# Optimization experiments

Hardware: AMD Instinct MI355X
Metric: run time of the kernel (lower is better)

## Reference

```python
import jax, jax.numpy as jnp
import numpy as np
import math

B, S, D = 2, 2048, 1024
H, DK, DV = 16, 64, 64  # head_count, query_size, value_size; H*DV == D
NEG_INF = -jnp.inf


def setup_inputs() -> dict:
    key = jax.random.key(0)
    ks = jax.random.split(key, 10)
    sc = 0.02
    return {
        "input": jax.random.normal(ks[0], (B, S, D), dtype=jnp.float32),
        "padding_mask": jnp.zeros((B, S), dtype=jnp.float32),  # 0 = valid, 1 = padded
        "wq_w": jax.random.normal(ks[1], (H * DK, D), dtype=jnp.float32) * sc,
        "wq_b": jnp.zeros((H * DK,), dtype=jnp.float32),
        "wk_w": jax.random.normal(ks[2], (H * DK, D), dtype=jnp.float32) * sc,
        "wk_b": jnp.zeros((H * DK,), dtype=jnp.float32),
        "wv_w": jax.random.normal(ks[3], (H * DV, D), dtype=jnp.float32) * sc,
        "wv_b": jnp.zeros((H * DV,), dtype=jnp.float32),
        "fin_w": jax.random.normal(ks[4], (D, H * DV), dtype=jnp.float32) * sc,
        "fin_b": jnp.zeros((D,), dtype=jnp.float32),
    }


def reference(input, padding_mask, wq_w, wq_b, wk_w, wk_b, wv_w, wv_b, fin_w, fin_b):
    b, s, _ = input.shape
    # projections -> [b, h, s, d]
    Q = (input @ wq_w.T + wq_b).reshape(b, s, H, DK).transpose(0, 2, 1, 3)
    K = (input @ wk_w.T + wk_b).reshape(b, s, H, DK).transpose(0, 2, 1, 3)
    V = (input @ wv_w.T + wv_b).reshape(b, s, H, DV).transpose(0, 2, 1, 3)

    # padding mask: pad*(-inf), nan_to_num(0*inf -> 0); broadcast over query dim
    pad = jnp.where(padding_mask > 0, NEG_INF, 0.0)[:, None, None, :]  # [b,1,1,s]
    i = jnp.arange(s)
    causal = jnp.where(i[None, :] < i[:, None] + 1, 0.0, NEG_INF)  # [s,s]
    mask = pad + causal[None, None, :, :]

    # (QK^T + mask) / sqrt(dk), softmax over keys
    logits = (jnp.einsum("bhqd,bhkd->bhqk", Q, K) + mask) / math.sqrt(DK)
    attn = jax.nn.softmax(logits, axis=-1)
    out = jnp.einsum("bhqk,bhkd->bqhd", attn, V).reshape(b, s, H * DV)
    return out @ fin_w.T + fin_b
```

## Files before the change

kernel.cpp:

```cpp
#include <hip/hip_runtime.h>


typedef __bf16 bf16;
typedef __bf16 bf16x4 __attribute__((ext_vector_type(4)));
typedef __bf16 bf16x8 __attribute__((ext_vector_type(8)));
typedef float  f32x4  __attribute__((ext_vector_type(4)));

#define B_  2
#define S_  2048
#define D_  1024
#define H_  16
#define HD  64
#define NEG_BIG (-3.0e38f)
#define SCALE_LOG2E 0.1803368801111204f

#define NSPLIT_QT 14
#define SLOTS_PER_BH (2 * NSPLIT_QT)

__device__ __forceinline__ void lds16(const void* g, void* l) {
    __builtin_amdgcn_global_load_lds((const __attribute__((address_space(1))) void*)g,
                                     (__attribute__((address_space(3))) void*)l, 16, 0, 0);
}

__device__ __forceinline__ f32x4 mfma16(bf16x8 a, bf16x8 b, f32x4 c) {
    return __builtin_amdgcn_mfma_f32_16x16x32_bf16(a, b, c, 0, 0, 0);
}

#define IT(qt, k0, ke) ((uint32_t)(qt) | ((uint32_t)(k0) << 8) | ((uint32_t)(ke) << 16))
__device__ __constant__ uint32_t g_items[46] = {
    IT(16,0,9),  IT(17,0,9),
    IT(30,0,8),  IT(30,8,16), IT(31,0,8),  IT(31,8,16),
    IT(28,0,8),  IT(29,0,8),  IT(14,0,8),  IT(15,0,8),
    IT(28,8,15), IT(29,8,15), IT(26,0,7),  IT(26,7,14),
    IT(27,0,7),  IT(27,7,14), IT(24,0,7),  IT(25,0,7),
    IT(12,0,7),  IT(13,0,7),
    IT(24,7,13), IT(25,7,13), IT(22,0,6),  IT(22,6,12),
    IT(23,0,6),  IT(23,6,12), IT(20,0,6),  IT(21,0,6),
    IT(10,0,6),  IT(11,0,6),
    IT(20,6,11), IT(21,6,11), IT(18,0,5),  IT(18,5,10),
    IT(19,0,5),  IT(19,5,10), IT(8,0,5),   IT(9,0,5),
    IT(6,0,4),   IT(7,0,4),
    IT(4,0,3),   IT(5,0,3),
    IT(2,0,2),   IT(3,0,2),
    IT(0,0,1),   IT(1,0,1)
};

__global__ __launch_bounds__(256) void convert_k(const float* __restrict__ X,
                                                 const float* __restrict__ wq,
                                                 const float* __restrict__ wk,
                                                 const float* __restrict__ wv,
                                                 const float* __restrict__ wo,
                                                 const float* __restrict__ pm,
                                                 bf16* __restrict__ dst,
                                                 bf16* __restrict__ validB) {
    const int gid = blockIdx.x * 256 + threadIdx.x;
    const int i   = gid * 4;
    const float* src;
    int off;
    if      (i < (4 << 20)) { src = X;  off = 0; }
    else if (i < (5 << 20)) { src = wq; off = 4 << 20; }
    else if (i < (6 << 20)) { src = wk; off = 5 << 20; }
    else if (i < (7 << 20)) { src = wv; off = 6 << 20; }
    else                    { src = wo; off = 7 << 20; }
    const float4 v = *(const float4*)(src + (i - off));
    bf16x4 p;
    p[0] = (bf16)v.x; p[1] = (bf16)v.y; p[2] = (bf16)v.z; p[3] = (bf16)v.w;
    *(bf16x4*)(dst + i) = p;
    if (gid < (B_ * S_) / 4) {
        const float4 m = *(const float4*)(pm + gid * 4);
        bf16x4 q;
        q[0] = (bf16)((m.x > 0.f) ? 0.f : 1.f);
        q[1] = (bf16)((m.y > 0.f) ? 0.f : 1.f);
        q[2] = (bf16)((m.z > 0.f) ? 0.f : 1.f);
        q[3] = (bf16)((m.w > 0.f) ? 0.f : 1.f);
        *(bf16x4*)(validB + gid * 4) = q;
    }
}

__global__ __launch_bounds__(256) void gemm_qkv(const bf16* __restrict__ A,
                                                const bf16* __restrict__ Wq,
                                                const bf16* __restrict__ Wk,
                                                const bf16* __restrict__ Wv,
                                                const float* __restrict__ bq,
                                                const float* __restrict__ bk,
                                                const float* __restrict__ bv,
                                                const float* __restrict__ pm,
                                                bf16* __restrict__ Qw,
                                                bf16* __restrict__ Kw,
                                                bf16* __restrict__ Vw) {
    constexpr int K = 1024;
    __shared__ bf16 sA[128 * 32];
    __shared__ bf16 sB[128 * 32];
    const int tid  = threadIdx.x;
    const int l15  = tid & 15;
    const int quad = (tid & 63) >> 4;
    const int wid  = tid >> 6;
    const int seg  = blockIdx.x >> 3;
    const int bn   = blockIdx.x & 7;
    const int bm   = blockIdx.y;
    const int wm   = (wid >> 1) * 64;
    const int wn   = (wid & 1) * 64;

    const bf16* W    = (seg == 0) ? Wq : (seg == 1) ? Wk : Wv;
    const float* bias = (seg == 0) ? bq : (seg == 1) ? bk : bv;

    const bf16* Ab = A + (size_t)bm * 128 * K;
    const bf16* Wb = W + (size_t)bn * 128 * K;

    f32x4 acc[4][4] = {};

    for (int k0 = 0; k0 < K; k0 += 32) {
        __syncthreads();
        #pragma unroll
        for (int it = 0; it < 2; ++it) {
            int c = it * 256 + tid;
            int row = c >> 2, c8 = c & 3;
            lds16(Ab + row * K + k0 + c8 * 8, (char*)sA + c * 16);
            lds16(Wb + row * K + k0 + c8 * 8, (char*)sB + c * 16);
        }
        __syncthreads();
        bf16x8 af[4], bfr[4];
        #pragma unroll
        for (int i = 0; i < 4; ++i)
            af[i] = *(const bf16x8*)&sA[(wm + i * 16 + l15) * 32 + quad * 8];
        #pragma unroll
        for (int i = 0; i < 4; ++i)
            bfr[i] = *(const bf16x8*)&sB[(wn + i * 16 + l15) * 32 + quad * 8];
        #pragma unroll
        for (int mi = 0; mi < 4; ++mi)
            #pragma unroll
            for (int ni = 0; ni < 4; ++ni)
                acc[mi][ni] = mfma16(af[mi], bfr[ni], acc[mi][ni]);
    }

    #pragma unroll
    for (int ni = 0; ni < 4; ++ni) {
        const int n  = bn * 128 + wn + ni * 16 + l15;
        const float bv_ = bias[n];
        const int h = n >> 6;
        #pragma unroll
        for (int mi = 0; mi < 4; ++mi) {
            const int m0 = bm * 128 + wm + mi * 16 + quad * 4;
            if (seg == 2) {
                const int dv = n & 63;
                const int b = m0 >> 11, s = m0 & 2047;
                const float4 pmv = *(const float4*)&pm[b * S_ + s];
                bf16x4 pack;
                #pragma unroll
                for (int r = 0; r < 4; ++r) {
                    const float vm = (((const float*)&pmv)[r] > 0.f) ? 0.f : 1.f;
                    pack[r] = (bf16)((acc[mi][ni][r] + bv_) * vm);
                }
                *(bf16x4*)&Vw[(((size_t)(b * H_ + h) * HD + dv) << 11) + s] = pack;
            } else {
                bf16* C = (seg == 0) ? Qw : Kw;
                const float qs = (seg == 0) ? SCALE_LOG2E : 1.0f;
                const int dk = n & 63;
                #pragma unroll
                for (int r = 0; r < 4; ++r) {
                    const int m = m0 + r, b = m >> 11, s = m & 2047;
                    C[(((size_t)(b * H_ + h) << 11) + s) * HD + dk] =
                        (bf16)((acc[mi][ni][r] + bv_) * qs);
                }
            }
        }
    }
}

__global__ __launch_bounds__(256) void gemm_fin(const bf16* __restrict__ A,
                                                const bf16* __restrict__ W,
                                                const float* __restrict__ bias,
                                                float* __restrict__ C) {
    constexpr int N = 1024, K = 1024;
    __shared__ bf16 sA[64 * 32];
    __shared__ bf16 sB[128 * 32];
    const int tid  = threadIdx.x;
    const int l15  = tid & 15;
    const int quad = (tid & 63) >> 4;
    const int wid  = tid >> 6;
    const int bm   = blockIdx.x >> 3;
    const int bn   = blockIdx.x & 7;
    const int wm   = (wid & 1) * 32;
    const int wn   = (wid >> 1) * 64;

    const bf16* Ab = A + (size_t)bm * 64 * K;
    const bf16* Wb = W + (size_t)bn * 128 * K;

    f32x4 acc[2][4] = {};

    for (int k0 = 0; k0 < K; k0 += 32) {
        __syncthreads();
        {
            int c = tid, row = c >> 2, c8 = c & 3;
            lds16(Ab + row * K + k0 + c8 * 8, (char*)sA + c * 16);
        }
        #pragma unroll
        for (int it = 0; it < 2; ++it) {
            int c = it * 256 + tid;
            int row = c >> 2, c8 = c & 3;
            lds16(Wb + row * K + k0 + c8 * 8, (char*)sB + c * 16);
        }
        __syncthreads();
        bf16x8 af[2], bfr[4];
        #pragma unroll
        for (int i = 0; i < 2; ++i)
            af[i] = *(const bf16x8*)&sA[(wm + i * 16 + l15) * 32 + quad * 8];
        #pragma unroll
        for (int i = 0; i < 4; ++i)
            bfr[i] = *(const bf16x8*)&sB[(wn + i * 16 + l15) * 32 + quad * 8];
        #pragma unroll
        for (int mi = 0; mi < 2; ++mi)
            #pragma unroll
            for (int ni = 0; ni < 4; ++ni)
                acc[mi][ni] = mfma16(af[mi], bfr[ni], acc[mi][ni]);
    }

    #pragma unroll
    for (int ni = 0; ni < 4; ++ni) {
        const int n  = bn * 128 + wn + ni * 16 + l15;
        const float bv = bias[n];
        #pragma unroll
        for (int mi = 0; mi < 2; ++mi) {
            const int m0 = bm * 64 + wm + mi * 16 + quad * 4;
            #pragma unroll
            for (int r = 0; r < 4; ++r)
                C[(size_t)(m0 + r) * N + n] = acc[mi][ni][r] + bv;
        }
    }
}

__global__ __launch_bounds__(256, 4) void attn_k(const bf16* __restrict__ Q,
                                                 const bf16* __restrict__ K,
                                                 const bf16* __restrict__ Vt,
                                                 const bf16* __restrict__ validB,
                                                 float* __restrict__ Opart,
                                                 float* __restrict__ Lpart,
                                                 bf16* __restrict__ Aout) {
    __shared__ bf16 sK_[2 * 128 * 32];
    __shared__ bf16 sV[4 * 64 * 32];
    const int tid  = threadIdx.x;
    const int l15  = tid & 15;
    const int quad = (tid & 63) >> 4;
    const int wid  = tid >> 6;
    const int bh   = blockIdx.x & 31;
    const int b    = bh >> 4;
    const int h    = bh & 15;

    const uint32_t itm = g_items[blockIdx.x >> 5];
    const int qt  = itm & 255;
    const int kt0 = (itm >> 8) & 255;
    const int kte = (itm >> 16) & 255;
    const int nkt = (qt >> 1) + 1;
    const bool split = (qt >= 18);

    const bf16* Qg = Q  + (size_t)bh * S_ * HD;
    const bf16* Kg = K  + (size_t)bh * S_ * HD;
    const bf16* Vg = Vt + (size_t)bh * HD * S_;
    const bf16* vB = validB + b * S_;

    bf16x8 qb[2];
    #pragma unroll
    for (int kk = 0; kk < 2; ++kk)
        qb[kk] = *(const bf16x8*)&Qg[(qt * 64 + wid * 16 + l15) * HD + kk * 32 + quad * 8];

    const int krow0 = (l15 >> 2) * 8 + (l15 & 3);
    const int qg    = qt * 64 + wid * 16 + l15;
    const int ckx = (quad ^ (((l15 >> 1) & 1) | (((l15 >> 2) & 1) << 1))) * 8;
    const int cvx = (quad ^ (((l15 >> 1) & 1) | (((l15 >> 3) & 1) << 1))) * 8;

    f32x4 o[4]  = {};
    f32x4 lacc  = {};

    for (int kt = kt0; kt < kte; ++kt) {
        __syncthreads();
        #pragma unroll
        for (int it = 0; it < 4; ++it) {
            int c = it * 256 + tid;
            { int pl = c >> 9, row = (c >> 2) & 127, c8 = c & 3;
              int sw = c8 ^ (((row >> 1) & 1) | (((row >> 3) & 1) << 1));
              lds16(Kg + ((size_t)kt * 128 + row) * HD + pl * 32 + sw * 8,
                    (char*)sK_ + c * 16); }
            { int kc = c >> 8, dv = (c >> 2) & 63, c8 = c & 3;
              int sw = c8 ^ (((dv >> 1) & 1) | (((dv >> 3) & 1) << 1));
              lds16(Vg + (size_t)kt * 128 + (size_t)dv * S_ + kc * 32 + sw * 8,
                    (char*)sV + c * 16); }
        }
        bf16x8 vf[4];
        #pragma unroll
        for (int g = 0; g < 4; ++g)
            vf[g] = *(const bf16x8*)&vB[kt * 128 + g * 32 + quad * 8];
        __syncthreads();

        const bool lastt = (kt == nkt - 1);
        #pragma unroll
        for (int g = 0; g < 4; ++g) {
            f32x4 s[2] = {};
            #pragma unroll
            for (int f = 0; f < 2; ++f)
                #pragma unroll
                for (int kk = 0; kk < 2; ++kk) {
                    bf16x8 ka = *(const bf16x8*)
                        &sK_[(kk * 128 + g * 32 + krow0 + f * 4) * 32 + ckx];
                    s[f] = mfma16(ka, qb[kk], s[f]);
                }
            bf16x8 pb;
            #pragma unroll
            for (int f = 0; f < 2; ++f)
                #pragma unroll
                for (int r = 0; r < 4; ++r) {
                    float v = s[f][r];
                    if (lastt && (kt * 128 + g * 32 + quad * 8 + f * 4 + r > qg))
                        v = NEG_BIG;
                    pb[f * 4 + r] = (bf16)exp2f(v);
                }
            lacc = mfma16(vf[g], pb, lacc);
            #pragma unroll
            for (int dvf = 0; dvf < 4; ++dvf) {
                bf16x8 va = *(const bf16x8*)
                    &sV[(g * 64 + dvf * 16 + l15) * 32 + cvx];
                o[dvf] = mfma16(va, pb, o[dvf]);
            }
        }
    }

    if (split) {
        const int sidx = (qt - 18) * 2 + (kt0 ? 1 : 0);
        const int slot = bh * SLOTS_PER_BH + sidx;
        const int q    = wid * 16 + l15;
        float* Ob = Opart + ((size_t)slot << 12) + q * 64 + quad * 4;
        #pragma unroll
        for (int dvf = 0; dvf < 4; ++dvf)
            *(f32x4*)(Ob + dvf * 16) = o[dvf];
        if (quad == 0) Lpart[slot * 64 + q] = lacc[0];
    } else {
        const float inv = 1.f / lacc[0];
        const size_t base = ((size_t)b * S_ + qg) * D_ + h * HD + quad * 4;
        #pragma unroll
        for (int dvf = 0; dvf < 4; ++dvf) {
            bf16x4 pk;
            #pragma unroll
            for (int r = 0; r < 4; ++r) pk[r] = (bf16)(o[dvf][r] * inv);
            *(bf16x4*)&Aout[base + dvf * 16] = pk;
        }
    }
}

__global__ __launch_bounds__(256) void combine_k(const float* __restrict__ Opart,
                                                 const float* __restrict__ Lpart,
                                                 bf16* __restrict__ Aw) {
    const int gid  = blockIdx.x * 256 + threadIdx.x;
    const int dc   = gid & 7;
    const int q    = (gid >> 3) & 63;
    const int rest = gid >> 9;
    const int qth  = rest % NSPLIT_QT;
    const int bh   = rest / NSPLIT_QT;
    const int slot0 = bh * SLOTS_PER_BH + qth * 2;
    const float l = Lpart[slot0 * 64 + q] + Lpart[(slot0 + 1) * 64 + q];
    const float inv = 1.f / l;
    const float* O0 = Opart + ((size_t)slot0 << 12) + q * 64 + dc * 8;
    const float* O1 = O0 + 4096;
    const float4 a0 = *(const float4*)O0;
    const float4 a1 = *(const float4*)(O0 + 4);
    const float4 b0 = *(const float4*)O1;
    const float4 b1 = *(const float4*)(O1 + 4);
    bf16x8 p;
    p[0] = (bf16)((a0.x + b0.x) * inv); p[1] = (bf16)((a0.y + b0.y) * inv);
    p[2] = (bf16)((a0.z + b0.z) * inv); p[3] = (bf16)((a0.w + b0.w) * inv);
    p[4] = (bf16)((a1.x + b1.x) * inv); p[5] = (bf16)((a1.y + b1.y) * inv);
    p[6] = (bf16)((a1.z + b1.z) * inv); p[7] = (bf16)((a1.w + b1.w) * inv);
    const int b = bh >> 4, h = bh & 15;
    const int s = (18 + qth) * 64 + q;
    *(bf16x8*)&Aw[((size_t)(b * S_ + s)) * D_ + h * HD + dc * 8] = p;
}

extern "C" void kernel_launch(void* const* d_in, const int* in_sizes, int n_in,
                              void* d_out, int out_size, void* d_ws, size_t ws_size,
                              hipStream_t stream) {
    const float* X   = (const float*)d_in[0];
    const float* pm  = (const float*)d_in[1];
    const float* wq  = (const float*)d_in[2];
    const float* bq  = (const float*)d_in[3];
    const float* wk  = (const float*)d_in[4];
    const float* bk  = (const float*)d_in[5];
    const float* wv  = (const float*)d_in[6];
    const float* bvb = (const float*)d_in[7];
    const float* wo  = (const float*)d_in[8];
    const float* bo  = (const float*)d_in[9];
    float* out = (float*)d_out;

    char* ws = (char*)d_ws;
    bf16* Xb  = (bf16*)(ws);
    bf16* Wqb = (bf16*)(ws + (8u  << 20));
    bf16* Wkb = (bf16*)(ws + (10u << 20));
    bf16* Wvb = (bf16*)(ws + (12u << 20));
    bf16* Wob = (bf16*)(ws + (14u << 20));
    bf16* Qw  = (bf16*)(ws + (16u << 20));
    bf16* Kw  = (bf16*)(ws + (24u << 20));
    bf16* Vw  = (bf16*)(ws + (32u << 20));
    bf16* Aw  = (bf16*)(ws + (40u << 20));
    float* Opart = (float*)(ws);
    bf16*  validB = (bf16*)(ws + (48u << 20));
    float* Lpart  = (float*)(ws + (48u << 20) + 65536);

    convert_k<<<dim3(8192), dim3(256), 0, stream>>>(X, wq, wk, wv, wo, pm,
                                                    Xb, validB);
    gemm_qkv<<<dim3(24, 32), dim3(256), 0, stream>>>(Xb, Wqb, Wkb, Wvb,
                                                     bq, bk, bvb, pm,
                                                     Qw, Kw, Vw);
    attn_k<<<dim3(1472), dim3(256), 0, stream>>>(Qw, Kw, Vw, validB,
                                                 Opart, Lpart, Aw);
    combine_k<<<dim3(896), dim3(256), 0, stream>>>(Opart, Lpart, Aw);
    gemm_fin<<<dim3(512), dim3(256), 0, stream>>>(Aw, Wob, bo, out);
}
```

Measured before the change: 207.7 us.

## Double-buffer LDS tiles and XOR-swizzle K chunks in projection GEMMs

Both projection GEMMs (QKV and final) now use two LDS buffers. The next K-slice is issued with global_load_lds before the MFMAs on the current slice, and one barrier per iteration replaces two. The 16-byte chunk position is also XOR-swizzled by row on the global side, with a matching swizzle on the LDS read, to reduce bank conflicts. This doubles shared memory per block. Correctness depends on the async LDS loads being complete at the single barrier, and there is no explicit vmcnt wait.

```diff
diff --git a/kernel.cpp b/kernel.cpp
--- a/kernel.cpp
+++ b/kernel.cpp
@@ -89,8 +89,8 @@
                                                 bf16* __restrict__ Kw,
                                                 bf16* __restrict__ Vw) {
     constexpr int K = 1024;
-    __shared__ bf16 sA[128 * 32];
-    __shared__ bf16 sB[128 * 32];
+    __shared__ bf16 sA[2][128 * 32];
+    __shared__ bf16 sB[2][128 * 32];
     const int tid  = threadIdx.x;
     const int l15  = tid & 15;
     const int quad = (tid & 63) >> 4;
@@ -108,30 +108,39 @@
     const bf16* Wb = W + (size_t)bn * 128 * K;
 
     f32x4 acc[4][4] = {};
-
+    const int rq = (quad ^ ((l15 >> 1) & 3)) * 8;
+
+#define QSTAGE(BUF, K0) do {                                                    \
+    _Pragma("unroll")                                                           \
+    for (int it_ = 0; it_ < 2; ++it_) {                                         \
+        int c_ = it_ * 256 + tid;                                               \
+        int row_ = c_ >> 2, c8_ = c_ & 3;                                       \
+        int sw_ = c8_ ^ ((row_ >> 1) & 3);                                      \
+        lds16(Ab + row_ * K + (K0) + sw_ * 8, (char*)sA[BUF] + c_ * 16);        \
+        lds16(Wb + row_ * K + (K0) + sw_ * 8, (char*)sB[BUF] + c_ * 16);        \
+    } } while (0)
+
+    QSTAGE(0, 0);
+    __syncthreads();
+    int cur = 0;
     for (int k0 = 0; k0 < K; k0 += 32) {
-        __syncthreads();
-        #pragma unroll
-        for (int it = 0; it < 2; ++it) {
-            int c = it * 256 + tid;
-            int row = c >> 2, c8 = c & 3;
-            lds16(Ab + row * K + k0 + c8 * 8, (char*)sA + c * 16);
-            lds16(Wb + row * K + k0 + c8 * 8, (char*)sB + c * 16);
-        }
-        __syncthreads();
+        if (k0 + 32 < K) QSTAGE(cur ^ 1, k0 + 32);
         bf16x8 af[4], bfr[4];
         #pragma unroll
         for (int i = 0; i < 4; ++i)
-            af[i] = *(const bf16x8*)&sA[(wm + i * 16 + l15) * 32 + quad * 8];
+            af[i] = *(const bf16x8*)&sA[cur][(wm + i * 16 + l15) * 32 + rq];
         #pragma unroll
         for (int i = 0; i < 4; ++i)
-            bfr[i] = *(const bf16x8*)&sB[(wn + i * 16 + l15) * 32 + quad * 8];
+            bfr[i] = *(const bf16x8*)&sB[cur][(wn + i * 16 + l15) * 32 + rq];
         #pragma unroll
         for (int mi = 0; mi < 4; ++mi)
             #pragma unroll
             for (int ni = 0; ni < 4; ++ni)
                 acc[mi][ni] = mfma16(af[mi], bfr[ni], acc[mi][ni]);
-    }
+        __syncthreads();
+        cur ^= 1;
+    }
+#undef QSTAGE
 
     #pragma unroll
     for (int ni = 0; ni < 4; ++ni) {
@@ -172,8 +181,8 @@
                                                 const float* __restrict__ bias,
                                                 float* __restrict__ C) {
     constexpr int N = 1024, K = 1024;
-    __shared__ bf16 sA[64 * 32];
-    __shared__ bf16 sB[128 * 32];
+    __shared__ bf16 sA[2][64 * 32];
+    __shared__ bf16 sB[2][128 * 32];
     const int tid  = threadIdx.x;
     const int l15  = tid & 15;
     const int quad = (tid & 63) >> 4;
@@ -187,33 +196,42 @@
     const bf16* Wb = W + (size_t)bn * 128 * K;
 
     f32x4 acc[2][4] = {};
-
+    const int rq = (quad ^ ((l15 >> 1) & 3)) * 8;
+
+#define FSTAGE(BUF, K0) do {                                                    \
+    {   int c_ = tid;                                                           \
+        int row_ = c_ >> 2, c8_ = c_ & 3;                                       \
+        int sw_ = c8_ ^ ((row_ >> 1) & 3);                                      \
+        lds16(Ab + row_ * K + (K0) + sw_ * 8, (char*)sA[BUF] + c_ * 16); }      \
+    _Pragma("unroll")                                                           \
+    for (int it_ = 0; it_ < 2; ++it_) {                                         \
+        int c_ = it_ * 256 + tid;                                               \
+        int row_ = c_ >> 2, c8_ = c_ & 3;                                       \
+        int sw_ = c8_ ^ ((row_ >> 1) & 3);                                      \
+        lds16(Wb + row_ * K + (K0) + sw_ * 8, (char*)sB[BUF] + c_ * 16);        \
+    } } while (0)
+
+    FSTAGE(0, 0);
+    __syncthreads();
+    int cur = 0;
     for (int k0 = 0; k0 < K; k0 += 32) {
-        __syncthreads();
-        {
-            int c = tid, row = c >> 2, c8 = c & 3;
-            lds16(Ab + row * K + k0 + c8 * 8, (char*)sA + c * 16);
-        }
-        #pragma unroll
-        for (int it = 0; it < 2; ++it) {
-            int c = it * 256 + tid;
-            int row = c >> 2, c8 = c & 3;
-            lds16(Wb + row * K + k0 + c8 * 8, (char*)sB + c * 16);
-        }
-        __syncthreads();
+        if (k0 + 32 < K) FSTAGE(cur ^ 1, k0 + 32);
         bf16x8 af[2], bfr[4];
         #pragma unroll
         for (int i = 0; i < 2; ++i)
-            af[i] = *(const bf16x8*)&sA[(wm + i * 16 + l15) * 32 + quad * 8];
+            af[i] = *(const bf16x8*)&sA[cur][(wm + i * 16 + l15) * 32 + rq];
         #pragma unroll
         for (int i = 0; i < 4; ++i)
-            bfr[i] = *(const bf16x8*)&sB[(wn + i * 16 + l15) * 32 + quad * 8];
+            bfr[i] = *(const bf16x8*)&sB[cur][(wn + i * 16 + l15) * 32 + rq];
         #pragma unroll
         for (int mi = 0; mi < 2; ++mi)
             #pragma unroll
             for (int ni = 0; ni < 4; ++ni)
                 acc[mi][ni] = mfma16(af[mi], bfr[ni], acc[mi][ni]);
-    }
+        __syncthreads();
+        cur ^= 1;
+    }
+#undef FSTAGE
 
     #pragma unroll
     for (int ni = 0; ni < 4; ++ni) {
```

Measured after the change: 197.9 us. 4.8% less time.
